# Kernel tuning notes

Hardware: AMD Instinct MI355X
Metric: run time of the kernel (lower is better)

Reference implementation:

```python
import jax, jax.numpy as jnp
import numpy as np

N = 32                      # rotation matrix size (n x n)
INPUT_DIM = 512
HIDDEN = 1024
BATCH = 16384
NUM_ANGLES = N * (N - 1) // 2   # 496

# Givens plane indices in the same order as the original double loop:
# i = 0..n-2, j = i+1..n-1 (row-major upper triangle)
_I_IDX, _J_IDX = np.triu_indices(N, k=1)


def setup_inputs() -> dict:
    key = jax.random.key(0)
    k0, k1, k2 = jax.random.split(key, 3)
    x = jax.random.normal(k0, (BATCH, INPUT_DIM), dtype=jnp.float32)
    # nn.Linear weights: fc (hidden, input_dim), fc2 (num_angles, hidden)
    W1 = jax.random.normal(k1, (HIDDEN, INPUT_DIM), dtype=jnp.float32) / np.sqrt(INPUT_DIM)
    b1 = jnp.zeros((HIDDEN,), dtype=jnp.float32)
    W2 = jax.random.normal(k2, (NUM_ANGLES, HIDDEN), dtype=jnp.float32) / np.sqrt(HIDDEN)
    b2 = jnpups = jnp.zeros((NUM_ANGLES,), dtype=jnp.float32)
    return {"x": x, "W1": W1, "b1": b1, "W2": W2, "b2": b2}


def reference(x, W1, b1, W2, b2):
    """Faithful forward: MLP -> angles -> sequential Givens-rotation product.

    Right-multiplying R by the Givens matrix G(i, j, theta) only mixes
    columns i and j of R, so each loop iteration is a 2-column update
    instead of a full [B, n, n] bmm. Same math as the original.
    """
    B = x.shape[0]
    h = jax.nn.relu(x @ W1.T + b1)                 # [B, HIDDEN]
    angles = jnp.mod(h @ W2.T + b2, 2.0 * jnp.pi)  # [B, NUM_ANGLES]
    c_all = jnp.cos(angles).T                      # [A, B]
    s_all = jnp.sin(angles).T                      # [A, B]

    R0 = jnp.tile(jnp.eye(N, dtype=x.dtype), (B, 1, 1))  # [B, n, n]
    i_idx = jnp.asarray(_I_IDX)
    j_idx = jnp.asarray(_J_IDX)

    def step(R, inp):
        i, j, c, s = inp                # scalars i, j; c, s: [B]
        col_i = R[:, :, i]              # [B, n]
        col_j = R[:, :, j]              # [B, n]
        new_i = col_i * c[:, None] + col_j * s[:, None]
        new_j = -col_i * s[:, None] + col_j * c[:, None]
        R = R.at[:, :, i].set(new_i)
        R = R.at[:, :, j].set(new_j)
        return R, None

    R, _ = jax.lax.scan(step, R0, (i_idx, j_idx, c_all, s_all))
    return R
```

## Files before the change

kernel.cpp:

```cpp
#include <hip/hip_runtime.h>
#include <math.h>
#include <utility>

#define BATCH 16384
#define INPUT_DIM 512
#define HIDDEN 1024
#define NROT 32
#define NANG 496

typedef _Float16 half8 __attribute__((ext_vector_type(8)));
typedef _Float16 half4 __attribute__((ext_vector_type(4)));
typedef float    f32x4 __attribute__((ext_vector_type(4)));
typedef float    f32x2 __attribute__((ext_vector_type(2)));

#define NX8  (BATCH * INPUT_DIM / 8)
#define NW18 (HIDDEN * INPUT_DIM / 8)
#define NW28 (512 * HIDDEN / 8)

__global__ __launch_bounds__(256) void prep_f16(
    const float* __restrict__ x, const float* __restrict__ W1,
    const float* __restrict__ W2, _Float16* __restrict__ x16,
    _Float16* __restrict__ W116, _Float16* __restrict__ W216)
{
    const int i = blockIdx.x * 256 + threadIdx.x;
    const float* src; _Float16* dst; int j; bool zero = false;
    if (i < NX8)              { j = i;               src = x;  dst = x16;  }
    else if (i < NX8 + NW18)  { j = i - NX8;         src = W1; dst = W116; }
    else if (i < NX8 + NW18 + NW28) {
        j = i - NX8 - NW18;   src = W2; dst = W216;
        zero = (j * 8 >= NANG * HIDDEN);
    } else return;

    half8 h;
    if (zero) {
        #pragma unroll
        for (int q = 0; q < 8; ++q) h[q] = (_Float16)0.f;
    } else {
        const float4* s = (const float4*)src + (size_t)j * 2;
        const float4 a = s[0], b = s[1];
        h[0]=(_Float16)a.x; h[1]=(_Float16)a.y; h[2]=(_Float16)a.z; h[3]=(_Float16)a.w;
        h[4]=(_Float16)b.x; h[5]=(_Float16)b.y; h[6]=(_Float16)b.z; h[7]=(_Float16)b.w;
    }
    *(half8*)(dst + (size_t)j * 8) = h;
}

__device__ __forceinline__ void gld16(const void* g, void* l) {
    __builtin_amdgcn_global_load_lds(
        (const __attribute__((address_space(1))) void*)g,
        (__attribute__((address_space(3))) void*)l, 16, 0, 0);
}

template<int EPI>
__global__ __launch_bounds__(256) void gemm_nt_f16(
    const _Float16* __restrict__ A, const _Float16* __restrict__ B,
    const float* __restrict__ bias, float* __restrict__ Cf,
    _Float16* __restrict__ Ch, int M, int K, int Nout, int GX)
{
    constexpr int BK = 32;
    __shared__ _Float16 sA[2][128 * BK];
    __shared__ _Float16 sB[2][128 * BK];

    const int g  = blockIdx.x;
    const int my = (g & 7) + (((g >> 3) / GX) << 3);
    const int mx = (g >> 3) % GX;
    const int m0 = my * 128;
    const int n0 = mx * 128;

    const int tid  = threadIdx.x;
    const int lane = tid & 63;
    const int wid  = tid >> 6;

    const int srow = lane >> 2;
    const int schk = (lane & 3) ^ (srow & 3);
    const _Float16* gA0 = A + (size_t)(m0 + wid * 32 + srow) * K + schk * 8;
    const _Float16* gA1 = gA0 + (size_t)16 * K;
    const _Float16* gB0 = B + (size_t)(n0 + wid * 32 + srow) * K + schk * 8;
    const _Float16* gB1 = gB0 + (size_t)16 * K;

    auto stage = [&](int kt, int buf) {
        const size_t ko = (size_t)kt * BK;
        gld16(gA0 + ko, &sA[buf][wid * 1024]);
        gld16(gA1 + ko, &sA[buf][wid * 1024 + 512]);
        gld16(gB0 + ko, &sB[buf][wid * 1024]);
        gld16(gB1 + ko, &sB[buf][wid * 1024 + 512]);
    };

    const int wr = wid >> 1, wc = wid & 1;
    const int fr = lane & 15, fq = lane >> 4;
    const int swR   = ((fq ^ (fr & 3)) << 3);
    const int aBase = (wr * 64 + fr) * BK + swR;
    const int bBase = (wc * 64 + fr) * BK + swR;

    f32x4 acc[4][4];
    #pragma unroll
    for (int i = 0; i < 4; ++i)
        #pragma unroll
        for (int j = 0; j < 4; ++j) acc[i][j] = (f32x4)(0.f);

    const int NT = K / BK;
    stage(0, 0);
    __syncthreads();
    int cur = 0;

    for (int kt = 0; kt < NT; ++kt) {
        if (kt + 1 < NT) stage(kt + 1, cur ^ 1);

        half8 a_[4], b_[4];
        #pragma unroll
        for (int f = 0; f < 4; ++f) {
            a_[f] = *(const half8*)&sA[cur][aBase + f * 16 * BK];
            b_[f] = *(const half8*)&sB[cur][bBase + f * 16 * BK];
        }
        #pragma unroll
        for (int fm = 0; fm < 4; ++fm)
            #pragma unroll
            for (int fn = 0; fn < 4; ++fn)
                acc[fm][fn] = __builtin_amdgcn_mfma_f32_16x16x32_f16(
                    a_[fm], b_[fn], acc[fm][fn], 0, 0, 0);

        __syncthreads();
        cur ^= 1;
    }

    if (EPI == 0) {
        #pragma unroll
        for (int fn = 0; fn < 4; ++fn) {
            const int col = n0 + wc * 64 + fn * 16 + fr;
            const float bv = bias[col];
            #pragma unroll
            for (int fm = 0; fm < 4; ++fm) {
                const int row0 = m0 + wr * 64 + fm * 16 + fq * 4;
                #pragma unroll
                for (int r = 0; r < 4; ++r)
                    Ch[(size_t)(row0 + r) * Nout + col] =
                        (_Float16)fmaxf(acc[fm][fn][r] + bv, 0.f);
            }
        }
    } else {
        #pragma unroll
        for (int fn = 0; fn < 4; ++fn) {
            const int col = n0 + wc * 64 + fn * 16 + fr;
            if (col < Nout) {
                const float bv = bias[col];
                #pragma unroll
                for (int fm = 0; fm < 4; ++fm) {
                    const int row0 = m0 + wr * 64 + fm * 16 + fq * 4;
                    #pragma unroll
                    for (int r = 0; r < 4; ++r)
                        Cf[(size_t)(row0 + r) * Nout + col] = acc[fm][fn][r] + bv;
                }
            }
        }
    }
}

struct IJTbl { unsigned char i[NANG]; unsigned char j[NANG]; };
constexpr IJTbl make_ij_tbl() {
    IJTbl t{};
    int k = 0;
    for (int i = 0; i < NROT - 1; ++i)
        for (int j = i + 1; j < NROT; ++j) { t.i[k] = (unsigned char)i; t.j[k] = (unsigned char)j; ++k; }
    return t;
}
constexpr IJTbl IJT = make_ij_tbl();

#define SLOT_H 1040
#define SLOT_F 520

__device__ __forceinline__ f32x2 lo2(const f32x4 q) { return __builtin_shufflevector(q, q, 0, 1); }
__device__ __forceinline__ f32x2 hi2(const f32x4 q) { return __builtin_shufflevector(q, q, 2, 3); }

template<int K, bool REV>
__device__ __forceinline__ void rot1pk(const f32x2 p, f32x2 (&v)[NROT]) {
    constexpr int i = IJT.i[K], j = IJT.j[K];
    f32x2 t0, t1, ni, nj;
    asm("v_pk_mul_f32 %0, %1, %2 op_sel:[1,0] op_sel_hi:[1,1]"
        : "=v"(t0) : "v"(p), "v"(v[j]));
    asm("v_pk_mul_f32 %0, %1, %2 op_sel:[1,0] op_sel_hi:[1,1]"
        : "=v"(t1) : "v"(p), "v"(v[i]));
    if constexpr (!REV) {
        asm("v_pk_fma_f32 %0, %1, %2, %3 op_sel:[0,0,0] op_sel_hi:[0,1,1]"
            : "=v"(ni) : "v"(p), "v"(v[i]), "v"(t0));
        asm("v_pk_fma_f32 %0, %1, %2, %3 op_sel:[0,0,0] op_sel_hi:[0,1,1] neg_lo:[0,0,1] neg_hi:[0,0,1]"
            : "=v"(nj) : "v"(p), "v"(v[j]), "v"(t1));
    } else {
        asm("v_pk_fma_f32 %0, %1, %2, %3 op_sel:[0,0,0] op_sel_hi:[0,1,1] neg_lo:[0,0,1] neg_hi:[0,0,1]"
            : "=v"(ni) : "v"(p), "v"(v[i]), "v"(t0));
        asm("v_pk_fma_f32 %0, %1, %2, %3 op_sel:[0,0,0] op_sel_hi:[0,1,1]"
            : "=v"(nj) : "v"(p), "v"(v[j]), "v"(t1));
    }
    v[i] = ni; v[j] = nj;
}

template<int W, int T>
__device__ __forceinline__ void chain_step(const float* __restrict__ lcs,
                                           f32x2 (&v)[NROT]) {
    if constexpr ((W & 1) == 0) {
        constexpr int g = T;
        constexpr int K0 = 124 * W + 2 * g;
        const f32x4 q = *(const f32x4*)(lcs + g * 4);
        rot1pk<K0,     false>(lo2(q), v);
        rot1pk<K0 + 1, false>(hi2(q), v);
    } else {
        constexpr int g = 61 - T;
        constexpr int K0 = 124 * W + 2 * g;
        const f32x4 q = *(const f32x4*)(lcs + g * 4);
        rot1pk<K0 + 1, true>(hi2(q), v);
        rot1pk<K0,     true>(lo2(q), v);
    }
}

template<int W, size_t... Ts>
__device__ __forceinline__ void chain_runW(const float* __restrict__ lcs,
                                           f32x2 (&v)[NROT],
                                           std::index_sequence<Ts...>) {
    (chain_step<W, (int)Ts>(lcs, v), ...);
}

template<int W>
__device__ __forceinline__ void chain_and_store(float* __restrict__ smemf,
                                                _Float16* __restrict__ lh,
                                                int b, int rp) {
    const float* lcs = smemf + (b * 4 + W) * SLOT_F;

    f32x2 v[NROT];
    #pragma unroll
    for (int c = 0; c < NROT; ++c) {
        f32x2 iv;
        iv[0] = (c == rp)      ? 1.f : 0.f;
        iv[1] = (c == rp + 16) ? 1.f : 0.f;
        v[c] = iv;
    }
    chain_runW<W>(lcs, v, std::make_index_sequence<62>{});

    const int base = (b * 4 + W) * SLOT_H;
    #pragma unroll
    for (int kq = 0; kq < 4; ++kq) {
        half8 h0, h1;
        #pragma unroll
        for (int j = 0; j < 8; ++j) {
            h0[j] = (_Float16)v[kq * 8 + j][0];
            h1[j] = (_Float16)v[kq * 8 + j][1];
        }
        const int sw = (kq ^ (rp & 3)) << 3;
        *(half8*)&lh[base +  rp       * 32 + sw] = h0;
        *(half8*)&lh[base + (rp + 16) * 32 + sw] = h1;
    }
}

__global__ __launch_bounds__(256) void rotate_kernel(
    const float* __restrict__ theta, float* __restrict__ out)
{
    __shared__ float smem[16 * SLOT_F];
    _Float16* lh = (_Float16*)smem;

    const int tid  = threadIdx.x;
    const int wid  = tid >> 6;
    const int lane = tid & 63;
    const int lb   = lane >> 4;
    const int rp   = lane & 15;
    const int fr = lane & 15, fq = lane >> 4;
    const size_t b0 = (size_t)blockIdx.x * 4;

    #pragma unroll
    for (int it = 0; it < 2; ++it) {
        const int t = it * 256 + tid;
        if (t < 496) {
            const int b    = t / 124;
            const int idx  = t - b * 124;
            const int w    = idx / 31;
            const int lidx = idx - 31 * w;
            const f32x4 th = *(const f32x4*)(theta + (b0 + b) * NANG + idx * 4);
            f32x4 p0, p1;
            float s, c;
            __sincosf(th[0], &s, &c); p0[0] = c; p0[1] = s;
            __sincosf(th[1], &s, &c); p0[2] = c; p0[3] = s;
            __sincosf(th[2], &s, &c); p1[0] = c; p1[1] = s;
            __sincosf(th[3], &s, &c); p1[2] = c; p1[3] = s;
            const int base = (b * 4 + w) * SLOT_F + lidx * 8;
            *(f32x4*)&smem[base]     = p0;
            *(f32x4*)&smem[base + 4] = p1;
        }
    }
    __syncthreads();

    if      (wid == 0) chain_and_store<0>(smem, lh, lb, rp);
    else if (wid == 1) chain_and_store<1>(smem, lh, lb, rp);
    else if (wid == 2) chain_and_store<2>(smem, lh, lb, rp);
    else               chain_and_store<3>(smem, lh, lb, rp);
    __syncthreads();

    {
        const int ba = wid;
        const int swz = (fq ^ (fr & 3)) << 3;
        half8 a[2][2], b[2][2];
        #pragma unroll
        for (int pi = 0; pi < 2; ++pi) {
            const int Asl = (pi == 0) ? (ba * 4 + 1) : (ba * 4 + 2);
            const int Bsl = (pi == 0) ? (ba * 4 + 0) : (ba * 4 + 3);
            #pragma unroll
            for (int mi = 0; mi < 2; ++mi) {
                a[pi][mi] = *(const half8*)&lh[Asl * SLOT_H + (mi * 16 + fr) * 32 + swz];
                b[pi][mi] = *(const half8*)&lh[Bsl * SLOT_H + (mi * 16 + fr) * 32 + swz];
            }
        }
        f32x4 d[2][2][2];
        #pragma unroll
        for (int pi = 0; pi < 2; ++pi)
            #pragma unroll
            for (int mi = 0; mi < 2; ++mi)
                #pragma unroll
                for (int ni = 0; ni < 2; ++ni)
                    d[pi][mi][ni] = __builtin_amdgcn_mfma_f32_16x16x32_f16(
                        a[pi][mi], b[pi][ni], (f32x4)(0.f), 0, 0, 0);
        __syncthreads();
        #pragma unroll
        for (int pi = 0; pi < 2; ++pi) {
            const int Pb = (ba * 4 + pi) * SLOT_H;
            #pragma unroll
            for (int mi = 0; mi < 2; ++mi)
                #pragma unroll
                for (int ni = 0; ni < 2; ++ni) {
                    half4 hv;
                    #pragma unroll
                    for (int q = 0; q < 4; ++q) hv[q] = (_Float16)d[pi][mi][ni][q];
                    const int col  = ni * 16 + fr;
                    const int rowb = (mi * 16 + fq * 4) ^ ((col & 3) << 3);
                    *(half4*)&lh[Pb + col * 32 + rowb] = hv;
                }
        }
    }
    __syncthreads();

    {
        const int ba = wid;
        const int Ab = (ba * 4 + 1) * SLOT_H;
        const int Bb = (ba * 4 + 0) * SLOT_H;
        const int Rb = (ba * 4 + 2) * SLOT_F;
        const int swz = (fq ^ (fr & 3)) << 3;
        #pragma unroll
        for (int mi = 0; mi < 2; ++mi) {
            const half8 a = *(const half8*)&lh[Ab + (mi * 16 + fr) * 32 + swz];
            #pragma unroll
            for (int ni = 0; ni < 2; ++ni) {
                const half8 b = *(const half8*)&lh[Bb + (ni * 16 + fr) * 32 + swz];
                const f32x4 d = __builtin_amdgcn_mfma_f32_16x16x32_f16(
                    a, b, (f32x4)(0.f), 0, 0, 0);
                const int row  = ni * 16 + fr;
                const int colq = mi * 4 + fq;
                *(f32x4*)&smem[Rb + row * 32 + ((colq ^ (row & 7)) << 2)] = d;
            }
        }
    }
    __syncthreads();

    #pragma unroll
    for (int s = 0; s < 4; ++s) {
        const int idx = s * 256 + tid;
        const int ba  = idx >> 8;
        const int f4i = idx & 255;
        const int row = f4i >> 3;
        const int cc  = f4i & 7;
        const f32x4 val =
            *(const f32x4*)&smem[(ba * 4 + 2) * SLOT_F + row * 32 + ((cc ^ (row & 7)) << 2)];
        *(f32x4*)(out + (b0 + ba) * 1024 + (size_t)f4i * 4) = val;
    }
}

extern "C" void kernel_launch(void* const* d_in, const int* in_sizes, int n_in,
                              void* d_out, int out_size, void* d_ws, size_t ws_size,
                              hipStream_t stream)
{
    const float* x  = (const float*)d_in[0];
    const float* W1 = (const float*)d_in[1];
    const float* b1 = (const float*)d_in[2];
    const float* W2 = (const float*)d_in[3];
    const float* b2 = (const float*)d_in[4];
    float* out = (float*)d_out;

    _Float16* h16  = (_Float16*)d_out;
    _Float16* x16  = h16  + (size_t)BATCH * HIDDEN;
    _Float16* W116 = x16  + (size_t)BATCH * INPUT_DIM;
    _Float16* W216 = W116 + (size_t)HIDDEN * INPUT_DIM;
    float*    th   = (float*)d_ws;

    prep_f16<<<dim3((NX8 + NW18 + NW28) / 256), 256, 0, stream>>>(
        x, W1, W2, x16, W116, W216);

    gemm_nt_f16<0><<<dim3(8 * 128), 256, 0, stream>>>(
        x16, W116, b1, nullptr, h16, BATCH, INPUT_DIM, HIDDEN, 8);

    gemm_nt_f16<1><<<dim3(4 * 128), 256, 0, stream>>>(
        h16, W216, b2, th, nullptr, BATCH, HIDDEN, NANG, 4);

    rotate_kernel<<<dim3(BATCH / 4), 256, 0, stream>>>(th, out);
}
```

Baseline: 103.6 us.

## Fuse fp32-to-fp16 conversion of x into first GEMM's A-tile loading

The first GEMM now reads x directly in fp32 through registers, converts it to fp16 and writes it into the swizzled LDS tile, so the prep kernel only converts the weights. This removes a full pass that wrote and re-read a fp16 copy of x (16 MB read, 8 MB write, 8 MB read). In exchange the A operand no longer uses the direct global-to-LDS load path, adds register pressure and does a second LDS write inside the loop, and each x row is read in fp32 by all 8 column tiles. The rotate kernel's shared-memory slot layout is also reindexed so slots are grouped by wave or stage instead of by batch.

```diff
diff --git a/kernel.cpp b/kernel.cpp
--- a/kernel.cpp
+++ b/kernel.cpp
@@ -13,21 +13,18 @@
 typedef float    f32x4 __attribute__((ext_vector_type(4)));
 typedef float    f32x2 __attribute__((ext_vector_type(2)));
 
-#define NX8  (BATCH * INPUT_DIM / 8)
 #define NW18 (HIDDEN * INPUT_DIM / 8)
 #define NW28 (512 * HIDDEN / 8)
 
-__global__ __launch_bounds__(256) void prep_f16(
-    const float* __restrict__ x, const float* __restrict__ W1,
-    const float* __restrict__ W2, _Float16* __restrict__ x16,
+__global__ __launch_bounds__(256) void prep_w16(
+    const float* __restrict__ W1, const float* __restrict__ W2,
     _Float16* __restrict__ W116, _Float16* __restrict__ W216)
 {
     const int i = blockIdx.x * 256 + threadIdx.x;
     const float* src; _Float16* dst; int j; bool zero = false;
-    if (i < NX8)              { j = i;               src = x;  dst = x16;  }
-    else if (i < NX8 + NW18)  { j = i - NX8;         src = W1; dst = W116; }
-    else if (i < NX8 + NW18 + NW28) {
-        j = i - NX8 - NW18;   src = W2; dst = W216;
+    if (i < NW18)             { j = i;          src = W1; dst = W116; }
+    else if (i < NW18 + NW28) {
+        j = i - NW18;           src = W2; dst = W216;
         zero = (j * 8 >= NANG * HIDDEN);
     } else return;
 
@@ -50,9 +47,9 @@
         (__attribute__((address_space(3))) void*)l, 16, 0, 0);
 }
 
-template<int EPI>
+template<int EPI, bool AF32>
 __global__ __launch_bounds__(256) void gemm_nt_f16(
-    const _Float16* __restrict__ A, const _Float16* __restrict__ B,
+    const void* __restrict__ Av, const _Float16* __restrict__ B,
     const float* __restrict__ bias, float* __restrict__ Cf,
     _Float16* __restrict__ Ch, int M, int K, int Nout, int GX)
 {
@@ -60,6 +57,9 @@
     __shared__ _Float16 sA[2][128 * BK];
     __shared__ _Float16 sB[2][128 * BK];
 
+    const _Float16* A16 = (const _Float16*)Av;
+    const float*    A32 = (const float*)Av;
+
     const int g  = blockIdx.x;
     const int my = (g & 7) + (((g >> 3) / GX) << 3);
     const int mx = (g >> 3) % GX;
@@ -71,18 +71,48 @@
     const int wid  = tid >> 6;
 
     const int srow = lane >> 2;
-    const int schk = (lane & 3) ^ (srow & 3);
-    const _Float16* gA0 = A + (size_t)(m0 + wid * 32 + srow) * K + schk * 8;
-    const _Float16* gA1 = gA0 + (size_t)16 * K;
+    const int sc   = lane & 3;
+    const int schk = sc ^ (srow & 3);
+
     const _Float16* gB0 = B + (size_t)(n0 + wid * 32 + srow) * K + schk * 8;
     const _Float16* gB1 = gB0 + (size_t)16 * K;
-
-    auto stage = [&](int kt, int buf) {
+    const _Float16* gA0 = A16 + (size_t)(m0 + wid * 32 + srow) * K + schk * 8;
+    const _Float16* gA1 = gA0 + (size_t)16 * K;
+    const float* fA0 = A32 + (size_t)(m0 + wid * 32 + srow) * K + sc * 8;
+    const float* fA1 = fA0 + (size_t)16 * K;
+
+    f32x4 ar[4];
+
+    auto stageB = [&](int kt, int buf) {
         const size_t ko = (size_t)kt * BK;
-        gld16(gA0 + ko, &sA[buf][wid * 1024]);
-        gld16(gA1 + ko, &sA[buf][wid * 1024 + 512]);
         gld16(gB0 + ko, &sB[buf][wid * 1024]);
         gld16(gB1 + ko, &sB[buf][wid * 1024 + 512]);
+        if constexpr (!AF32) {
+            gld16(gA0 + ko, &sA[buf][wid * 1024]);
+            gld16(gA1 + ko, &sA[buf][wid * 1024 + 512]);
+        }
+    };
+    auto loadA = [&](int kt) {
+        if constexpr (AF32) {
+            const size_t ko = (size_t)kt * BK;
+            ar[0] = *(const f32x4*)(fA0 + ko);
+            ar[1] = *(const f32x4*)(fA0 + ko + 4);
+            ar[2] = *(const f32x4*)(fA1 + ko);
+            ar[3] = *(const f32x4*)(fA1 + ko + 4);
+        }
+    };
+    auto writeA = [&](int buf) {
+        if constexpr (AF32) {
+            half8 h0, h1;
+            #pragma unroll
+            for (int j = 0; j < 4; ++j) {
+                h0[j] = (_Float16)ar[0][j]; h0[4 + j] = (_Float16)ar[1][j];
+                h1[j] = (_Float16)ar[2][j]; h1[4 + j] = (_Float16)ar[3][j];
+            }
+            const int r0 = wid * 32 + srow;
+            *(half8*)&sA[buf][ r0       * 32 + (schk << 3)] = h0;
+            *(half8*)&sA[buf][(r0 + 16) * 32 + (schk << 3)] = h1;
+        }
     };
 
     const int wr = wid >> 1, wc = wid & 1;
@@ -98,12 +128,15 @@
         for (int j = 0; j < 4; ++j) acc[i][j] = (f32x4)(0.f);
 
     const int NT = K / BK;
-    stage(0, 0);
+    loadA(0);
+    stageB(0, 0);
+    writeA(0);
     __syncthreads();
     int cur = 0;
 
     for (int kt = 0; kt < NT; ++kt) {
-        if (kt + 1 < NT) stage(kt + 1, cur ^ 1);
+        const bool more = (kt + 1 < NT);
+        if (more) { loadA(kt + 1); stageB(kt + 1, cur ^ 1); }
 
         half8 a_[4], b_[4];
         #pragma unroll
@@ -118,6 +151,7 @@
                 acc[fm][fn] = __builtin_amdgcn_mfma_f32_16x16x32_f16(
                     a_[fm], b_[fn], acc[fm][fn], 0, 0, 0);
 
+        if (more) writeA(cur ^ 1);
         __syncthreads();
         cur ^= 1;
     }
@@ -166,6 +200,7 @@
 
 #define SLOT_H 1040
 #define SLOT_F 520
+#define R_BASE (8 * SLOT_F)
 
 __device__ __forceinline__ f32x2 lo2(const f32x4 q) { return __builtin_shufflevector(q, q, 0, 1); }
 __device__ __forceinline__ f32x2 hi2(const f32x4 q) { return __builtin_shufflevector(q, q, 2, 3); }
@@ -221,7 +256,7 @@
 __device__ __forceinline__ void chain_and_store(float* __restrict__ smemf,
                                                 _Float16* __restrict__ lh,
                                                 int b, int rp) {
-    const float* lcs = smemf + (b * 4 + W) * SLOT_F;
+    const float* lcs = smemf + (W * 4 + b) * SLOT_F;
 
     f32x2 v[NROT];
     #pragma unroll
@@ -233,7 +268,7 @@
     }
     chain_runW<W>(lcs, v, std::make_index_sequence<62>{});
 
-    const int base = (b * 4 + W) * SLOT_H;
+    const int base = (W * 4 + b) * SLOT_H;
     #pragma unroll
     for (int kq = 0; kq < 4; ++kq) {
         half8 h0, h1;
@@ -277,7 +312,7 @@
             __sincosf(th[1], &s, &c); p0[2] = c; p0[3] = s;
             __sincosf(th[2], &s, &c); p1[0] = c; p1[1] = s;
             __sincosf(th[3], &s, &c); p1[2] = c; p1[3] = s;
-            const int base = (b * 4 + w) * SLOT_F + lidx * 8;
+            const int base = (w * 4 + b) * SLOT_F + lidx * 8;
             *(f32x4*)&smem[base]     = p0;
             *(f32x4*)&smem[base + 4] = p1;
         }
@@ -296,8 +331,8 @@
         half8 a[2][2], b[2][2];
         #pragma unroll
         for (int pi = 0; pi < 2; ++pi) {
-            const int Asl = (pi == 0) ? (ba * 4 + 1) : (ba * 4 + 2);
-            const int Bsl = (pi == 0) ? (ba * 4 + 0) : (ba * 4 + 3);
+            const int Asl = (pi == 0) ? (4 + ba)  : (8 + ba);
+            const int Bsl = (pi == 0) ? (ba)      : (12 + ba);
             #pragma unroll
             for (int mi = 0; mi < 2; ++mi) {
                 a[pi][mi] = *(const half8*)&lh[Asl * SLOT_H + (mi * 16 + fr) * 32 + swz];
@@ -316,7 +351,7 @@
         __syncthreads();
         #pragma unroll
         for (int pi = 0; pi < 2; ++pi) {
-            const int Pb = (ba * 4 + pi) * SLOT_H;
+            const int Pb = (pi * 4 + ba) * SLOT_H;
             #pragma unroll
             for (int mi = 0; mi < 2; ++mi)
                 #pragma unroll
@@ -334,9 +369,9 @@
 
     {
         const int ba = wid;
-        const int Ab = (ba * 4 + 1) * SLOT_H;
-        const int Bb = (ba * 4 + 0) * SLOT_H;
-        const int Rb = (ba * 4 + 2) * SLOT_F;
+        const int Ab = (4 + ba) * SLOT_H;
+        const int Bb = (ba)     * SLOT_H;
+        const int Rb = R_BASE + ba * 1032;
         const int swz = (fq ^ (fr & 3)) << 3;
         #pragma unroll
         for (int mi = 0; mi < 2; ++mi) {
@@ -362,7 +397,7 @@
         const int row = f4i >> 3;
         const int cc  = f4i & 7;
         const f32x4 val =
-            *(const f32x4*)&smem[(ba * 4 + 2) * SLOT_F + row * 32 + ((cc ^ (row & 7)) << 2)];
+            *(const f32x4*)&smem[R_BASE + ba * 1032 + row * 32 + ((cc ^ (row & 7)) << 2)];
         *(f32x4*)(out + (b0 + ba) * 1024 + (size_t)f4i * 4) = val;
     }
 }
@@ -379,18 +414,16 @@
     float* out = (float*)d_out;
 
     _Float16* h16  = (_Float16*)d_out;
-    _Float16* x16  = h16  + (size_t)BATCH * HIDDEN;
-    _Float16* W116 = x16  + (size_t)BATCH * INPUT_DIM;
+    _Float16* W116 = h16  + (size_t)BATCH * HIDDEN;
     _Float16* W216 = W116 + (size_t)HIDDEN * INPUT_DIM;
     float*    th   = (float*)d_ws;
 
-    prep_f16<<<dim3((NX8 + NW18 + NW28) / 256), 256, 0, stream>>>(
-        x, W1, W2, x16, W116, W216);
-
-    gemm_nt_f16<0><<<dim3(8 * 128), 256, 0, stream>>>(
-        x16, W116, b1, nullptr, h16, BATCH, INPUT_DIM, HIDDEN, 8);
-
-    gemm_nt_f16<1><<<dim3(4 * 128), 256, 0, stream>>>(
+    prep_w16<<<dim3((NW18 + NW28) / 256), 256, 0, stream>>>(W1, W2, W116, W216);
+
+    gemm_nt_f16<0, true><<<dim3(8 * 128), 256, 0, stream>>>(
+        x, W116, b1, nullptr, h16, BATCH, INPUT_DIM, HIDDEN, 8);
+
+    gemm_nt_f16<1, false><<<dim3(4 * 128), 256, 0, stream>>>(
         h16, W216, b2, th, nullptr, BATCH, HIDDEN, NANG, 4);
 
     rotate_kernel<<<dim3(BATCH / 4), 256, 0, stream>>>(th, out);
```

Result: no change. 104.8 us (+1.2%).
